# Performance work log

Measured on AMD Instinct MI355X. Metric: run time of the kernel, lower is better.

Reference implementation:

```python
import jax, jax.numpy as jnp
import numpy as np

IN_Q, OUT_Q = 32, 32
GRID_H, GRID_W = 64, 64
FREQ_H, FREQ_W = GRID_H, GRID_W // 2 + 1
BATCH = 32
INIT_SCALE = 0.02


def setup_inputs() -> dict:
    key = jax.random.key(0)
    keys = jax.random.split(key, 9)
    inp = {"x": jax.random.normal(keys[0], (BATCH, 4 * IN_Q, GRID_H, GRID_W), dtype=jnp.float32)}
    names = ["kr_w", "kr_x", "kr_y", "kr_z", "ki_w", "ki_x", "ki_y", "ki_z"]
    for i, n in enumerate(names):
        inp[n] = jax.random.normal(keys[i + 1], (IN_Q, OUT_Q, FREQ_H, FREQ_W), dtype=jnp.float32) * INIT_SCALE
    return inp


def reference(x, kr_w, kr_x, kr_y, kr_z, ki_w, ki_x, ki_y, ki_z):
    q = IN_Q
    # Split quaternion components and FFT each: [B, q, H, Wf] complex
    xs = jnp.stack([x[:, :q], x[:, q:2 * q], x[:, 2 * q:3 * q], x[:, 3 * q:]])  # [4,B,q,H,W]
    Xs = jnp.fft.rfft2(xs, s=(GRID_H, GRID_W), axes=(-2, -1))  # [4,B,q,H,Wf]
    # Complex kernels, stacked: [4, in_q, out_q, H, Wf]
    Ws = jnp.stack([kr_w + 1j * ki_w, kr_x + 1j * ki_x, kr_y + 1j * ki_y, kr_z + 1j * ki_z])
    # All 16 pairwise contractions in one einsum: C[p,q] = W_p contracted with X_q
    C = jnp.einsum('piohw,qbihw->pqbohw', Ws, Xs)  # [4,4,B,out,H,Wf]
    # Hamilton product combination
    Pw = C[0, 0] - C[1, 1] - C[2, 2] - C[3, 3]
    Px = C[0, 1] + C[1, 0] + C[2, 3] - C[3, 2]
    Py = C[0, 2] - C[1, 3] + C[2, 0] + C[3, 1]
    Pz = C[0, 3] + C[1, 2] - C[2, 1] + C[3, 0]
    P = jnp.stack([Pw, Px, Py, Pz])  # [4,B,out,H,Wf]
    o = jnp.fft.irfft2(P, s=(GRID_H, GRID_W), axes=(-2, -1))  # [4,B,out,H,W]
    # cat along channel dim: [B, 4*out, H, W]
    return jnp.concatenate([o[0], o[1], o[2], o[3]], axis=1)
```

## Files before the change

### kernel.cpp

```cpp
#include <hip/hip_runtime.h>

#define FH 64
#define FW 64
#define NWF 33
#define NBIN (FH*NWF)
#define NIMG 4096
#define PI2 6.283185307179586f

typedef unsigned short u16;
typedef unsigned int u32;
typedef __attribute__((ext_vector_type(8))) short bf16x8;
typedef __attribute__((ext_vector_type(8))) _Float16 f16x8;
typedef __attribute__((ext_vector_type(4))) unsigned short u16x4;
typedef __attribute__((ext_vector_type(4))) float f32x4;
typedef __attribute__((ext_vector_type(4))) int   i32x4;

__device__ __forceinline__ u16 f2bf(float f) {
    unsigned u = __float_as_uint(f);
    unsigned r = (u + 0x7FFFu + ((u >> 16) & 1u)) >> 16;
    return (u16)r;
}
__device__ __forceinline__ u16 f2h(float f) {
    _Float16 h = (_Float16)f;
    return __builtin_bit_cast(u16, h);
}
__device__ __forceinline__ float2 upk(u32 v) {
    return make_float2(__uint_as_float(v << 16), __uint_as_float(v & 0xFFFF0000u));
}
__device__ __forceinline__ u32 pk(float2 v) {
    return (u32)f2bf(v.x) | ((u32)f2bf(v.y) << 16);
}
__device__ __forceinline__ f16x8 negh(f16x8 v) {
    i32x4 t = __builtin_bit_cast(i32x4, v);
    t ^= (int)0x80008000;
    return __builtin_bit_cast(f16x8, t);
}

__global__ __launch_bounds__(512, 4) void fwd_prep_kernel(
    const float* __restrict__ x, u32* __restrict__ Xs,
    const float* __restrict__ s0, const float* __restrict__ s1,
    const float* __restrict__ s2, const float* __restrict__ s3,
    const float* __restrict__ s4, const float* __restrict__ s5,
    const float* __restrict__ s6, const float* __restrict__ s7,
    u16* __restrict__ WT)
{
    __shared__ __align__(16) u16 sm[36864];
    const int tid = threadIdx.x;

    if (blockIdx.x < 1024) {
        const int lane = tid & 63;
        const int wid  = tid >> 6;
        const int slot = wid >> 1;
        const int half = wid & 1;
        const int a16  = lane & 15;
        const int q    = lane >> 4;

        const int img = blockIdx.x * 4 + slot;
        const int qc = img >> 10;
        const int b  = (img >> 5) & 31;
        const int ci = img & 31;
        const float* __restrict__ src = x + ((size_t)b*128 + (size_t)qc*32 + ci) * (FH*FW);

        u16* mats0 = sm;
        u16* mats1 = sm + 64*72;
        u16* ST    = sm + 9216 + slot*6912;

        for (int t = tid; t < 4096; t += 512) {
            int a = t >> 6, bb = t & 63;
            float sn, cs;
            __sincosf(PI2 * (float)((a*bb) & 63) * (1.f/64.f), &sn, &cs);
            mats0[a*72 + bb] = f2h(cs);
            mats1[a*72 + bb] = f2h(sn);
        }

        f16x8 xf[2][2];
        #pragma unroll
        for (int mtl = 0; mtl < 2; ++mtl)
            #pragma unroll
            for (int ks = 0; ks < 2; ++ks) {
                const float* rp = src + (16*(2*half + mtl) + a16)*64 + ks*32 + q*8;
                float4 v0 = *(const float4*)rp;
                float4 v1 = *(const float4*)(rp + 4);
                xf[mtl][ks] = (f16x8){ (_Float16)v0.x, (_Float16)v0.y, (_Float16)v0.z, (_Float16)v0.w,
                                       (_Float16)v1.x, (_Float16)v1.y, (_Float16)v1.z, (_Float16)v1.w };
            }
        __syncthreads();

        #pragma unroll
        for (int mtl = 0; mtl < 2; ++mtl) {
            const int mt = 2*half + mtl;
            f32x4 are[3], aim[3];
            #pragma unroll
            for (int nt = 0; nt < 3; ++nt) { are[nt] = (f32x4){0,0,0,0}; aim[nt] = (f32x4){0,0,0,0}; }
            #pragma unroll
            for (int nt = 0; nt < 3; ++nt)
                #pragma unroll
                for (int ks = 0; ks < 2; ++ks) {
                    const int rb = (16*nt + a16)*72 + ks*32 + q*8;
                    f16x8 cf = *(const f16x8*)&mats0[rb];
                    f16x8 sf = *(const f16x8*)&mats1[rb];
                    are[nt] = __builtin_amdgcn_mfma_f32_16x16x32_f16(xf[mtl][ks], cf, are[nt], 0, 0, 0);
                    aim[nt] = __builtin_amdgcn_mfma_f32_16x16x32_f16(xf[mtl][ks], negh(sf), aim[nt], 0, 0, 0);
                }
            const int hb = 16*mt + 4*q;
            #pragma unroll
            for (int nt = 0; nt < 3; ++nt) {
                u16x4 re4 = { f2h(are[nt][0]), f2h(are[nt][1]), f2h(are[nt][2]), f2h(are[nt][3]) };
                u16x4 im4 = { f2h(aim[nt][0]), f2h(aim[nt][1]), f2h(aim[nt][2]), f2h(aim[nt][3]) };
                *(u16x4*)&ST[(16*nt + a16)*72 + hb]      = re4;
                *(u16x4*)&ST[(48 + 16*nt + a16)*72 + hb] = im4;
            }
        }
        __syncthreads();

        f16x8 bfr[2][3][2];
        #pragma unroll
        for (int ri = 0; ri < 2; ++ri)
            #pragma unroll
            for (int nt = 0; nt < 3; ++nt)
                #pragma unroll
                for (int ks = 0; ks < 2; ++ks)
                    bfr[ri][nt][ks] = *(const f16x8*)&ST[(ri*48 + 16*nt + a16)*72 + ks*32 + q*8];

        u32* __restrict__ dst = Xs + (size_t)img * NBIN;
        #pragma unroll
        for (int mtl = 0; mtl < 2; ++mtl) {
            const int mt = 2*half + mtl;
            f16x8 cfa[2], sfa[2], nsf[2];
            #pragma unroll
            for (int ks = 0; ks < 2; ++ks) {
                const int rb = (16*mt + a16)*72 + ks*32 + q*8;
                cfa[ks] = *(const f16x8*)&mats0[rb];
                sfa[ks] = *(const f16x8*)&mats1[rb];
                nsf[ks] = negh(sfa[ks]);
            }
            #pragma unroll
            for (int nt = 0; nt < 3; ++nt) {
                f32x4 xre = (f32x4){0,0,0,0}, xim = (f32x4){0,0,0,0};
                #pragma unroll
                for (int ks = 0; ks < 2; ++ks) {
                    xre = __builtin_amdgcn_mfma_f32_16x16x32_f16(cfa[ks], bfr[0][nt][ks], xre, 0, 0, 0);
                    xre = __builtin_amdgcn_mfma_f32_16x16x32_f16(sfa[ks], bfr[1][nt][ks], xre, 0, 0, 0);
                    xim = __builtin_amdgcn_mfma_f32_16x16x32_f16(cfa[ks], bfr[1][nt][ks], xim, 0, 0, 0);
                    xim = __builtin_amdgcn_mfma_f32_16x16x32_f16(nsf[ks], bfr[0][nt][ks], xim, 0, 0, 0);
                }
                const int k = 16*nt + a16;
                if (k < 33) {
                    #pragma unroll
                    for (int r = 0; r < 4; ++r)
                        dst[(16*mt + 4*q + r)*33 + k] = pk(make_float2(xre[r], xim[r]));
                }
            }
        }
    } else {
        const int pb = blockIdx.x - 1024;
        const int bt = pb % 66;
        const int ay = pb / 66;
        const int a  = ay >> 2;
        const int o0 = (ay & 3) * 8;
        const float* __restrict__ src =
            (a==0)?s0:(a==1)?s1:(a==2)?s2:(a==3)?s3:(a==4)?s4:(a==5)?s5:(a==6)?s6:s7;
        const int bin0 = bt * 32;
        u16* lds2 = sm;

        #pragma unroll
        for (int it = 0; it < 4; ++it) {
            int e = tid + it*512;
            int f4 = e & 7, rt = e >> 3;
            int i = rt & 31, oo = rt >> 5;
            int io = i*32 + o0 + oo;
            float4 v = ((const float4*)src)[(size_t)io*(NBIN/4) + bt*8 + f4];
            int chL = oo*32 + i;
            int bb = f4*4;
            lds2[(bb+0)*264 + chL] = f2bf(v.x);
            lds2[(bb+1)*264 + chL] = f2bf(v.y);
            lds2[(bb+2)*264 + chL] = f2bf(v.z);
            lds2[(bb+3)*264 + chL] = f2bf(v.w);
        }
        __syncthreads();
        const int p = a & 3, ri = a >> 2;
        #pragma unroll
        for (int it = 0; it < 2; ++it) {
            int e = tid + it*512;
            int binL = e >> 5, c8 = e & 31;
            bf16x8 v = *(const bf16x8*)&lds2[binL*264 + c8*8];
            size_t d = ((size_t)(bin0 + binL)*8 + p*2 + ri)*1024 + o0*32 + c8*8;
            *(bf16x8*)(WT + d) = v;
        }
    }
}

__global__ __launch_bounds__(256) void xpose_x_kernel(const u32* __restrict__ Xs,
                                                      u32* __restrict__ XT)
{
    const int g    = blockIdx.x;
    const int bin0 = blockIdx.y * 32;
    __shared__ u32 tile[32][33];
    const int tid = threadIdx.x;
    #pragma unroll
    for (int it = 0; it < 4; ++it) {
        int e = tid + it*256;
        int imgL = e >> 5, binL = e & 31;
        tile[imgL][binL] = Xs[(size_t)(g*32 + imgL) * NBIN + bin0 + binL];
    }
    __syncthreads();
    const int q = g >> 5, b = g & 31;
    #pragma unroll
    for (int it = 0; it < 2; ++it) {
        int e = tid + it*256;
        int binL = e >> 4, pr = e & 15;
        u32 v0 = tile[pr*2][binL], v1 = tile[pr*2 + 1][binL];
        u32 re = (v0 & 0xFFFFu) | (v1 << 16);
        u32 im = (v0 >> 16) | (v1 & 0xFFFF0000u);
        size_t base = ((size_t)(bin0 + binL)*8 + q*2) * 512 + b*16 + pr;
        XT[base]       = re;
        XT[base + 512] = im;
    }
}

__global__ __launch_bounds__(256) void contract_kernel(
    const u16* __restrict__ XT, const u16* __restrict__ WT,
    u32* __restrict__ P)
{
    const int bid  = blockIdx.x;
    const int bin  = (bid & 7) * (NBIN/8) + (bid >> 3);
    const int wid  = threadIdx.x >> 6;
    const int lane = threadIdx.x & 63;
    const int bh = wid >> 1, oh = wid & 1;
    const int row = lane & 15, kg = lane >> 4;

    const u16* __restrict__ xb = XT + (size_t)bin * 8192;
    const u16* __restrict__ wb = WT + (size_t)bin * 8192;

    bf16x8 ax[4][2];
    #pragma unroll
    for (int q = 0; q < 4; ++q)
        #pragma unroll
        for (int ri = 0; ri < 2; ++ri)
            ax[q][ri] = *(const bf16x8*)(xb + ((q*2 + ri)*32 + bh*16 + row)*32 + kg*8);

    bf16x8 wpos[4][2], wneg[4][2];
    #pragma unroll
    for (int p = 0; p < 4; ++p)
        #pragma unroll
        for (int ri = 0; ri < 2; ++ri) {
            bf16x8 w = *(const bf16x8*)(wb + ((p*2 + ri)*32 + oh*16 + row)*32 + kg*8);
            wpos[p][ri] = w;
            i32x4 t = __builtin_bit_cast(i32x4, w);
            t ^= (int)0x80008000;
            wneg[p][ri] = __builtin_bit_cast(bf16x8, t);
        }

    f32x4 acc[4][2];
    #pragma unroll
    for (int c = 0; c < 4; ++c)
        #pragma unroll
        for (int ri = 0; ri < 2; ++ri)
            acc[c][ri] = (f32x4){0.f, 0.f, 0.f, 0.f};

    constexpr int PI_[4][4] = {{0,1,2,3},{1,0,3,2},{2,3,0,1},{3,2,1,0}};
    constexpr int SG_[4][4] = {{1,-1,-1,-1},{1,1,-1,1},{1,1,1,-1},{1,-1,1,1}};
    #pragma unroll
    for (int c = 0; c < 4; ++c)
        #pragma unroll
        for (int q = 0; q < 4; ++q) {
            const int  p   = PI_[c][q];
            const bool pos = SG_[c][q] > 0;
            bf16x8 wr_s = pos ? wpos[p][0] : wneg[p][0];
            bf16x8 wi_s = pos ? wpos[p][1] : wneg[p][1];
            bf16x8 wi_m = pos ? wneg[p][1] : wpos[p][1];
            acc[c][0] = __builtin_amdgcn_mfma_f32_16x16x32_bf16(ax[q][0], wr_s, acc[c][0], 0, 0, 0);
            acc[c][0] = __builtin_amdgcn_mfma_f32_16x16x32_bf16(ax[q][1], wi_m, acc[c][0], 0, 0, 0);
            acc[c][1] = __builtin_amdgcn_mfma_f32_16x16x32_bf16(ax[q][1], wr_s, acc[c][1], 0, 0, 0);
            acc[c][1] = __builtin_amdgcn_mfma_f32_16x16x32_bf16(ax[q][0], wi_s, acc[c][1], 0, 0, 0);
        }

    u32* __restrict__ dst = P + (size_t)bin * 4096;
    #pragma unroll
    for (int c = 0; c < 4; ++c)
        #pragma unroll
        for (int r = 0; r < 4; ++r) {
            int b_ = bh*16 + kg*4 + r;
            int o  = oh*16 + row;
            dst[c*1024 + b_*32 + o] = pk(make_float2(acc[c][0][r], acc[c][1][r]));
        }
}

__global__ __launch_bounds__(256) void pxpose_kernel(const u32* __restrict__ P,
                                                     u32* __restrict__ PT)
{
    const int bin0 = blockIdx.x * 32;
    const int img0 = blockIdx.y * 32;
    __shared__ u32 tile[32][33];
    const int tid = threadIdx.x;
    #pragma unroll
    for (int it = 0; it < 4; ++it) {
        int e = tid + it*256;
        int bi = e >> 5, im = e & 31;
        tile[bi][im] = P[(size_t)(bin0 + bi) * 4096 + img0 + im];
    }
    __syncthreads();
    #pragma unroll
    for (int it = 0; it < 4; ++it) {
        int e = tid + it*256;
        int im = e >> 5, bi = e & 31;
        PT[(size_t)(img0 + im) * NBIN + bin0 + bi] = tile[bi][im];
    }
}

__global__ __launch_bounds__(512, 4) void fft_inv_kernel(const u32* __restrict__ PT,
                                                         float* __restrict__ out)
{
    __shared__ __align__(16) u16 mats[2][64*72];
    __shared__ __align__(16) u16 wbuf[4][7168];

    const int tid  = threadIdx.x;
    const int lane = tid & 63;
    const int wid  = tid >> 6;
    const int slot = wid >> 1;
    const int half = wid & 1;
    const int ltid = (half << 6) | lane;
    const int a16  = lane & 15;
    const int q    = lane >> 4;

    const int img = blockIdx.x * 4 + slot;
    const int c  = img >> 10;
    const int b  = (img >> 5) & 31;
    const int oc = img & 31;

    for (int t = tid; t < 4096; t += 512) {
        int a = t >> 6, bb = t & 63;
        float sn, cs;
        __sincosf(PI2 * (float)((a*bb) & 63) * (1.f/64.f), &sn, &cs);
        mats[0][a*72 + bb] = f2h(cs);
        mats[1][a*72 + bb] = f2h(sn);
    }

    u16* ETre = wbuf[slot];
    u16* ETim = wbuf[slot] + 48*72;
    for (int j = 33*72 + ltid; j < 48*72; j += 128) {
        ETre[j] = 0;
        ETim[j] = 0;
    }
    const u32* __restrict__ srcP = PT + (size_t)img * NBIN;
    for (int i = 0; i < 17; ++i) {
        int t = i*128 + ltid;
        if (t < NBIN) {
            int hf = t / 33, k = t - hf*33;
            float2 v = upk(srcP[t]);
            ETre[k*72 + hf] = f2h(v.x);
            ETim[k*72 + hf] = f2h(v.y);
        }
    }
    __syncthreads();

    f16x8 ere[2][2], eim[2][2];
    #pragma unroll
    for (int mtl = 0; mtl < 2; ++mtl) {
        const int mt = 2*half + mtl;
        if (mt < 3) {
            #pragma unroll
            for (int ks = 0; ks < 2; ++ks) {
                ere[mtl][ks] = *(const f16x8*)&ETre[(16*mt + a16)*72 + ks*32 + q*8];
                eim[mtl][ks] = *(const f16x8*)&ETim[(16*mt + a16)*72 + ks*32 + q*8];
            }
        }
    }
    __syncthreads();

    u16* Tre = wbuf[slot];
    u16* Tim = wbuf[slot] + 64*56;
    #pragma unroll
    for (int mtl = 0; mtl < 2; ++mtl) {
        const int mt = 2*half + mtl;
        if (mt < 3) {
            #pragma unroll
            for (int nt = 0; nt < 4; ++nt) {
                f32x4 tre = (f32x4){0,0,0,0}, tim = (f32x4){0,0,0,0};
                #pragma unroll
                for (int ks = 0; ks < 2; ++ks) {
                    const int rb = (16*nt + a16)*72 + ks*32 + q*8;
                    f16x8 cf = *(const f16x8*)&mats[0][rb];
                    f16x8 sf = *(const f16x8*)&mats[1][rb];
                    tre = __builtin_amdgcn_mfma_f32_16x16x32_f16(ere[mtl][ks], cf, tre, 0, 0, 0);
                    tre = __builtin_amdgcn_mfma_f32_16x16x32_f16(eim[mtl][ks], negh(sf), tre, 0, 0, 0);
                    tim = __builtin_amdgcn_mfma_f32_16x16x32_f16(ere[mtl][ks], sf, tim, 0, 0, 0);
                    tim = __builtin_amdgcn_mfma_f32_16x16x32_f16(eim[mtl][ks], cf, tim, 0, 0, 0);
                }
                const int m0 = 16*mt + 4*q;
                u16x4 r4, i4;
                #pragma unroll
                for (int r = 0; r < 4; ++r) {
                    int m = m0 + r;
                    float s = (m == 0 || m == 32) ? (1.f/4096.f) : (2.f/4096.f);
                    r4[r] = (m < 33) ? f2h(tre[r] * s) : (u16)0;
                    i4[r] = (m < 33) ? f2h(tim[r] * s) : (u16)0;
                }
                *(u16x4*)&Tre[(16*nt + a16)*56 + m0] = r4;
                *(u16x4*)&Tim[(16*nt + a16)*56 + m0] = i4;
            }
        }
    }
    __syncthreads();

    float* __restrict__ dst = out + ((size_t)b*128 + (size_t)c*32 + oc) * (FH*FW);
    #pragma unroll
    for (int mtl = 0; mtl < 2; ++mtl) {
        const int mt = 2*half + mtl;
        f16x8 tfr[2], tfi[2];
        #pragma unroll
        for (int ks = 0; ks < 2; ++ks) {
            const int mbase = ks*32 + q*8;
            if (mbase < 48) {
                tfr[ks] = *(const f16x8*)&Tre[(16*mt + a16)*56 + mbase];
                tfi[ks] = *(const f16x8*)&Tim[(16*mt + a16)*56 + mbase];
            } else {
                tfr[ks] = (f16x8){0,0,0,0,0,0,0,0};
                tfi[ks] = (f16x8){0,0,0,0,0,0,0,0};
            }
        }
        #pragma unroll
        for (int nt = 0; nt < 4; ++nt) {
            f32x4 acc = (f32x4){0,0,0,0};
            #pragma unroll
            for (int ks = 0; ks < 2; ++ks) {
                const int rb = (16*nt + a16)*72 + ks*32 + q*8;
                f16x8 cf = *(const f16x8*)&mats[0][rb];
                f16x8 sf = *(const f16x8*)&mats[1][rb];
                acc = __builtin_amdgcn_mfma_f32_16x16x32_f16(tfr[ks], cf, acc, 0, 0, 0);
                acc = __builtin_amdgcn_mfma_f32_16x16x32_f16(tfi[ks], negh(sf), acc, 0, 0, 0);
            }
            #pragma unroll
            for (int r = 0; r < 4; ++r)
                dst[(16*mt + 4*q + r)*64 + 16*nt + a16] = acc[r];
        }
    }
}

extern "C" void kernel_launch(void* const* d_in, const int* in_sizes, int n_in,
                              void* d_out, int out_size, void* d_ws, size_t ws_size,
                              hipStream_t stream)
{
    const float* x   = (const float*)d_in[0];
    const float* krw = (const float*)d_in[1];
    const float* krx = (const float*)d_in[2];
    const float* kry = (const float*)d_in[3];
    const float* krz = (const float*)d_in[4];
    const float* kiw = (const float*)d_in[5];
    const float* kix = (const float*)d_in[6];
    const float* kiy = (const float*)d_in[7];
    const float* kiz = (const float*)d_in[8];

    const size_t R = (size_t)NBIN * 8192 * sizeof(u16);
    u16* XT = (u16*)d_ws;
    u32* PT = (u32*)d_ws;
    u16* WT = (u16*)((char*)d_ws + R);
    u32* Xs = (u32*)((char*)d_ws + 2*R);
    u32* P  = Xs;
    float* out = (float*)d_out;

    fwd_prep_kernel<<<dim3(1024 + 2112), 512, 0, stream>>>(x, Xs,
                                                           krw, krx, kry, krz,
                                                           kiw, kix, kiy, kiz, WT);
    xpose_x_kernel<<<dim3(128, NBIN/32), 256, 0, stream>>>(Xs, (u32*)XT);
    contract_kernel<<<dim3(NBIN), 256, 0, stream>>>(XT, WT, P);
    pxpose_kernel<<<dim3(NBIN/32, NIMG/32), 256, 0, stream>>>(P, PT);
    fft_inv_kernel<<<dim3(NIMG/4), 512, 0, stream>>>(PT, out);
}
```

Before: 112.6 us.

## Fuse P transpose into inverse FFT kernel with swizzled block-to-image mapping

Drops the separate pxpose kernel. The inverse FFT now gathers each of its four images straight from the bin-major P buffer, reading 4 contiguous u32 per bin, which removes one full write and read of the P intermediate and one launch. Blocks are remapped with a swizzle so that blocks running at the same time touch neighbouring image groups and share cache lines. The reads are strided by 16KB per bin, with only 16 bytes used per row, so cache efficiency relies on L2 and MALL hits across concurrent blocks.

```diff
diff --git a/kernel.cpp b/kernel.cpp
--- a/kernel.cpp
+++ b/kernel.cpp
@@ -286,29 +286,7 @@
         }
 }
 
-__global__ __launch_bounds__(256) void pxpose_kernel(const u32* __restrict__ P,
-                                                     u32* __restrict__ PT)
-{
-    const int bin0 = blockIdx.x * 32;
-    const int img0 = blockIdx.y * 32;
-    __shared__ u32 tile[32][33];
-    const int tid = threadIdx.x;
-    #pragma unroll
-    for (int it = 0; it < 4; ++it) {
-        int e = tid + it*256;
-        int bi = e >> 5, im = e & 31;
-        tile[bi][im] = P[(size_t)(bin0 + bi) * 4096 + img0 + im];
-    }
-    __syncthreads();
-    #pragma unroll
-    for (int it = 0; it < 4; ++it) {
-        int e = tid + it*256;
-        int im = e >> 5, bi = e & 31;
-        PT[(size_t)(img0 + im) * NBIN + bin0 + bi] = tile[bi][im];
-    }
-}
-
-__global__ __launch_bounds__(512, 4) void fft_inv_kernel(const u32* __restrict__ PT,
+__global__ __launch_bounds__(512, 4) void fft_inv_kernel(const u32* __restrict__ P,
                                                          float* __restrict__ out)
 {
     __shared__ __align__(16) u16 mats[2][64*72];
@@ -323,7 +301,9 @@
     const int a16  = lane & 15;
     const int q    = lane >> 4;
 
-    const int img = blockIdx.x * 4 + slot;
+    const int bid = blockIdx.x;
+    const int g   = (bid & 7) * 128 + (bid >> 3);
+    const int img = g * 4 + slot;
     const int c  = img >> 10;
     const int b  = (img >> 5) & 31;
     const int oc = img & 31;
@@ -336,24 +316,28 @@
         mats[1][a*72 + bb] = f2h(sn);
     }
 
+    {
+        u16* ETre = wbuf[slot];
+        u16* ETim = wbuf[slot] + 48*72;
+        for (int j = 33*72 + ltid; j < 48*72; j += 128) {
+            ETre[j] = 0;
+            ETim[j] = 0;
+        }
+    }
+    for (int e = tid; e < NBIN*4; e += 512) {
+        int bin = e >> 2, sl = e & 3;
+        u32 v = P[(size_t)bin * 4096 + g*4 + sl];
+        float2 f = upk(v);
+        int hf = bin / 33, k = bin - hf*33;
+        u16* ETre = wbuf[sl];
+        u16* ETim = wbuf[sl] + 48*72;
+        ETre[k*72 + hf] = f2h(f.x);
+        ETim[k*72 + hf] = f2h(f.y);
+    }
+    __syncthreads();
+
     u16* ETre = wbuf[slot];
     u16* ETim = wbuf[slot] + 48*72;
-    for (int j = 33*72 + ltid; j < 48*72; j += 128) {
-        ETre[j] = 0;
-        ETim[j] = 0;
-    }
-    const u32* __restrict__ srcP = PT + (size_t)img * NBIN;
-    for (int i = 0; i < 17; ++i) {
-        int t = i*128 + ltid;
-        if (t < NBIN) {
-            int hf = t / 33, k = t - hf*33;
-            float2 v = upk(srcP[t]);
-            ETre[k*72 + hf] = f2h(v.x);
-            ETim[k*72 + hf] = f2h(v.y);
-        }
-    }
-    __syncthreads();
-
     f16x8 ere[2][2], eim[2][2];
     #pragma unroll
     for (int mtl = 0; mtl < 2; ++mtl) {
@@ -453,7 +437,6 @@
 
     const size_t R = (size_t)NBIN * 8192 * sizeof(u16);
     u16* XT = (u16*)d_ws;
-    u32* PT = (u32*)d_ws;
     u16* WT = (u16*)((char*)d_ws + R);
     u32* Xs = (u32*)((char*)d_ws + 2*R);
     u32* P  = Xs;
@@ -464,6 +447,5 @@
                                                            kiw, kix, kiy, kiz, WT);
     xpose_x_kernel<<<dim3(128, NBIN/32), 256, 0, stream>>>(Xs, (u32*)XT);
     contract_kernel<<<dim3(NBIN), 256, 0, stream>>>(XT, WT, P);
-    pxpose_kernel<<<dim3(NBIN/32, NIMG/32), 256, 0, stream>>>(P, PT);
-    fft_inv_kernel<<<dim3(NIMG/4), 512, 0, stream>>>(PT, out);
-}
+    fft_inv_kernel<<<dim3(NIMG/4), 512, 0, stream>>>(P, out);
+}
```

New measurement: 102.8 us. 8.8% less time.
